# Kernel tuning notes

Measured on AMD Instinct MI355X. Metric: run time of the kernel, lower is better.

The kernel has to match this reference:

```python
import math
import jax, jax.numpy as jnp
import numpy as np

B, T = 2, 2048
D_MODEL, D_HEAD = 2048, 128
N_Q, N_KV = 16, 4
QPG = N_Q // N_KV  # queries per kv group
ROPE_BASE = 10000.0
YARN_SCALE = 4.0
ORIG_MAX_LEN = 4096
BETA_FAST, BETA_SLOW = 32.0, 1.0
RMS_EPS = 1.1920929e-07  # torch.finfo(float32).eps (nn.RMSNorm default)


def _yarn_inv_freq():
    inv = 1.0 / ROPE_BASE ** (np.arange(0, D_HEAD, 2, dtype=np.float32) / D_HEAD)
    wavelengths = 2.0 * math.pi / inv
    low_wavelen = ORIG_MAX_LEN / BETA_SLOW
    high_wavelen = ORIG_MAX_LEN / BETA_FAST
    gamma = np.clip((low_wavelen - wavelengths) / (low_wavelen - high_wavelen), 0.0, 1.0)
    return (gamma * inv + (1.0 - gamma) * inv / YARN_SCALE).astype(np.float32)

INV_FREQ = jnp.asarray(_yarn_inv_freq())  # (D_HEAD//2,) constant buffer
MSCALE = 0.1 * math.log(YARN_SCALE) + 1.0
ATTN_SCALE = 1.0 / (MSCALE * math.sqrt(D_HEAD))


def _rms_norm(x, w):
    # normalize over last dim (d_head), learnable per-dim weight
    return x * jax.lax.rsqrt(jnp.mean(x * x, axis=-1, keepdims=True) + RMS_EPS) * w


def _apply_rope(x):
    # x: (..., T, d_head)
    t = jnp.arange(x.shape[-2], dtype=jnp.float32)
    freqs = jnp.outer(t, INV_FREQ)                 # (T, d/2)
    emb = jnp.concatenate([freqs, freqs], axis=-1)  # (T, d)
    cos, sin = jnp.cos(emb), jnp.sin(emb)
    half = x.shape[-1] // 2
    x_rot = jnp.concatenate([-x[..., half:], x[..., :half]], axis=-1)
    return x * cos + x_rot * sin


def setup_inputs() -> dict:
    key = jax.random.key(0)
    ks = jax.random.split(key, 5)
    x = jax.random.normal(ks[0], (B, T, D_MODEL), dtype=jnp.float32)
    w_scale = 0.02
    Wq = jax.random.normal(ks[1], (D_MODEL, N_Q * D_HEAD), dtype=jnp.float32) * w_scale
    Wkv = jax.random.normal(ks[2], (D_MODEL, 2 * N_KV * D_HEAD), dtype=jnp.float32) * w_scale
    Wo = jax.random.normal(ks[3], (N_Q * D_HEAD, D_MODEL), dtype=jnp.float32) * w_scale
    q_norm_w = jnp.ones((D_HEAD,), dtype=jnp.float32)
    k_norm_w = jnp.ones((D_HEAD,), dtype=jnp.float32)
    return {"x": x, "Wq": Wq, "Wkv": Wkv, "Wo": Wo,
            "q_norm_w": q_norm_w, "k_norm_w": k_norm_w}


def reference(x, Wq, Wkv, Wo, q_norm_w, k_norm_w):
    b, t, _ = x.shape
    # projections
    q = (x @ Wq).reshape(b, t, QPG, N_KV, D_HEAD).transpose(0, 2, 3, 1, 4)  # (b,qpg,g,t,d)
    kv = x @ Wkv
    k, v = jnp.split(kv, 2, axis=-1)
    k = k.reshape(b, t, N_KV, D_HEAD).transpose(0, 2, 1, 3)  # (b,g,t,d)
    v = v.reshape(b, t, N_KV, D_HEAD).transpose(0, 2, 1, 3)  # (b,g,t,d)
    # RMSNorm + YaRN RoPE on q,k (math done in float32 as in source)
    q = _apply_rope(_rms_norm(q, q_norm_w))
    k = _apply_rope(_rms_norm(k, k_norm_w))
    # GQA replication: head index h = qpg*N_KV + g (matches source rearrange/reshape)
    q = q.reshape(b, N_Q, t, D_HEAD)
    k = jnp.broadcast_to(k[:, None], (b, QPG, N_KV, t, D_HEAD)).reshape(b, N_Q, t, D_HEAD)
    v = jnp.broadcast_to(v[:, None], (b, QPG, N_KV, t, D_HEAD)).reshape(b, N_Q, t, D_HEAD)
    # causal SDPA with custom scale
    scores = jnp.einsum('bhtd,bhsd->bhts', q, k) * ATTN_SCALE
    causal = jnp.tril(jnp.ones((t, t), dtype=bool))
    scores = jnp.where(causal, scores, jnp.finfo(scores.dtype).min)
    probs = jax.nn.softmax(scores, axis=-1)
    attn = jnp.einsum('bhts,bhsd->bhtd', probs, v)
    out = attn.transpose(0, 2, 1, 3).reshape(b, t, N_Q * D_HEAD)
    return out @ Wo
```

## Files before the change

kernel.cpp:

```cpp
#include <hip/hip_runtime.h>
#include <cmath>

typedef float f32x4 __attribute__((ext_vector_type(4)));
typedef __bf16 bf16x8 __attribute__((ext_vector_type(8)));

#define DEV static __device__ __forceinline__

DEV unsigned short f2bf(float f) {
  unsigned int u = __builtin_bit_cast(unsigned int, f);
  u += 0x7FFFu + ((u >> 16) & 1u);
  return (unsigned short)(u >> 16);
}
DEV float bf2f(unsigned short h) {
  unsigned int u = ((unsigned int)h) << 16;
  return __builtin_bit_cast(float, u);
}
DEV unsigned int cvtpk(float lo, float hi) {
  unsigned int r;
  asm("v_cvt_pk_bf16_f32 %0, %1, %2" : "=v"(r) : "v"(lo), "v"(hi));
  return r;
}
DEV f32x4 mfma16(bf16x8 a, bf16x8 b, f32x4 c) {
  return __builtin_amdgcn_mfma_f32_16x16x32_bf16(a, b, c, 0, 0, 0);
}
DEV void dma16(const void* g, void* l) {
  __builtin_amdgcn_global_load_lds(
      (const __attribute__((address_space(1))) void*)(uintptr_t)g,
      (__attribute__((address_space(3))) void*)(unsigned int)(uintptr_t)l,
      16, 0, 0);
}

constexpr int T_SEQ = 2048;

__global__ __launch_bounds__(256) void build_rope(float2* __restrict__ rope) {
  int gid = blockIdx.x * 256 + threadIdx.x;
  if (gid >= T_SEQ * 64) return;
  int t = gid >> 6, i = gid & 63;
  double inv = pow(10000.0, -((double)(2 * i)) / 128.0);
  double wl = 6.283185307179586 / inv;
  double gm = (4096.0 - wl) / (4096.0 - 128.0);
  gm = gm < 0.0 ? 0.0 : (gm > 1.0 ? 1.0 : gm);
  float f = (float)(gm * inv + (1.0 - gm) * inv * 0.25);
  float th = (float)t * f;
  float s, c;
  sincosf(th, &s, &c);
  rope[gid] = make_float2(c, s);
}

__global__ __launch_bounds__(256) void cvt_f32_bf16(const float4* __restrict__ in,
                                                    ushort* __restrict__ out, int n4) {
  int i = blockIdx.x * 256 + threadIdx.x;
  if (i >= n4) return;
  float4 v = in[i];
  unsigned int lo = (unsigned int)f2bf(v.x) | ((unsigned int)f2bf(v.y) << 16);
  unsigned int hi = (unsigned int)f2bf(v.z) | ((unsigned int)f2bf(v.w) << 16);
  int row = i >> 9;
  int e = (i * 4) & 2047;
  size_t o = ((size_t)row << 11) + (size_t)(e ^ ((row & 7) << 3));
  *(uint2*)(out + o) = make_uint2(lo, hi);
}

__global__ __launch_bounds__(256) void tconv(const float* __restrict__ in,
                                             ushort* __restrict__ out, int R, int C) {
  __shared__ ushort tile[64][65];
  int c0 = blockIdx.x * 64, r0 = blockIdx.y * 64;
  int j = threadIdx.x & 63, i0 = threadIdx.x >> 6;
#pragma unroll
  for (int ii = 0; ii < 16; ++ii) {
    int i = i0 + ii * 4;
    tile[i][j] = f2bf(in[(size_t)(r0 + i) * C + c0 + j]);
  }
  __syncthreads();
#pragma unroll
  for (int ii = 0; ii < 16; ++ii) {
    int jr = i0 + ii * 4;
    out[(size_t)(c0 + jr) * R + ((r0 + j) ^ ((jr & 7) << 3))] = tile[j][jr];
  }
}

template <int OUT_BF16>
__global__ __launch_bounds__(256) void gemm_bt(const ushort* __restrict__ A,
                                               const ushort* __restrict__ Bt,
                                               void* __restrict__ Cv,
                                               int M, int N, int K) {
  __shared__ ushort lA[128 * 64];
  __shared__ ushort lB[128 * 64];
  const int tid = threadIdx.x;
  const int lane = tid & 63;
  const int w = tid >> 6;
  const int m0 = blockIdx.y * 128;
  const int n0 = blockIdx.x * 128;
  const int wm = (w >> 1) << 6;
  const int wn = (w & 1) << 6;

  f32x4 acc[4][4] = {};

  const size_t K2 = (size_t)K * 2;
  const char* Ab = (const char*)A + (size_t)m0 * K2;
  const char* Bb = (const char*)Bt + (size_t)n0 * K2;
  const int drow = w * 32 + (lane >> 3);
  const int dcb = (lane & 7) * 16;

  for (int k0 = 0; k0 < K; k0 += 64) {
#pragma unroll
    for (int ii = 0; ii < 4; ++ii) {
      const int off = w * 4096 + ii * 1024;
      const size_t gofs = (size_t)(drow + ii * 8) * K2 + (size_t)k0 * 2 + dcb;
      dma16(Ab + gofs, (char*)lA + off);
      dma16(Bb + gofs, (char*)lB + off);
    }
    __syncthreads();
#pragma unroll
    for (int kc = 0; kc < 2; ++kc) {
      bf16x8 a[4], bb[4];
#pragma unroll
      for (int mt = 0; mt < 4; ++mt) {
        int row = wm + mt * 16 + (lane & 15);
        int byo = kc * 64 + ((lane >> 4) << 4);
        a[mt] = *(const bf16x8*)((const char*)lA + row * 128 + (byo ^ ((row & 7) << 4)));
      }
#pragma unroll
      for (int nt = 0; nt < 4; ++nt) {
        int row = wn + nt * 16 + (lane & 15);
        int byo = kc * 64 + ((lane >> 4) << 4);
        bb[nt] = *(const bf16x8*)((const char*)lB + row * 128 + (byo ^ ((row & 7) << 4)));
      }
#pragma unroll
      for (int mt = 0; mt < 4; ++mt)
#pragma unroll
        for (int nt = 0; nt < 4; ++nt)
          acc[mt][nt] = mfma16(a[mt], bb[nt], acc[mt][nt]);
    }
    __syncthreads();
  }

  const int rr = (lane >> 4) << 2;
  const int cc = lane & 15;
  if (OUT_BF16) {
    ushort* C = (ushort*)Cv;
#pragma unroll
    for (int mt = 0; mt < 4; ++mt)
#pragma unroll
      for (int nt = 0; nt < 4; ++nt)
#pragma unroll
        for (int j = 0; j < 4; ++j) {
          int r = m0 + wm + mt * 16 + rr + j;
          int c = n0 + wn + nt * 16 + cc;
          C[(size_t)r * N + c] = f2bf(acc[mt][nt][j]);
        }
  } else {
    float* C = (float*)Cv;
#pragma unroll
    for (int mt = 0; mt < 4; ++mt)
#pragma unroll
      for (int nt = 0; nt < 4; ++nt)
#pragma unroll
        for (int j = 0; j < 4; ++j) {
          int r = m0 + wm + mt * 16 + rr + j;
          int c = n0 + wn + nt * 16 + cc;
          C[(size_t)r * N + c] = acc[mt][nt][j];
        }
  }
}

__global__ __launch_bounds__(256) void norm_rope(const ushort* __restrict__ qkv,
                                                 const float* __restrict__ qw,
                                                 const float* __restrict__ kw,
                                                 const float2* __restrict__ rope,
                                                 ushort* __restrict__ qout,
                                                 ushort* __restrict__ kout,
                                                 float q_scale) {
  const int w = threadIdx.x >> 6, lane = threadIdx.x & 63;
  const int vi = blockIdx.x * 4 + w;
  const ushort* src;
  const float* wt;
  ushort* dst;
  float extra;
  int t, bb;
  if (vi < 65536) {
    int row = vi >> 4, H = vi & 15;
    bb = row >> 11;
    t = row & 2047;
    src = qkv + (size_t)row * 3072 + H * 128 + lane * 2;
    wt = qw;
    extra = q_scale;
    dst = qout + ((size_t)(bb * 16 + H) * T_SEQ + t) * 128 + lane * 2;
  } else {
    int vi2 = vi - 65536;
    int row = vi2 >> 2, gg = vi2 & 3;
    bb = row >> 11;
    t = row & 2047;
    src = qkv + (size_t)row * 3072 + 2048 + gg * 128 + lane * 2;
    wt = kw;
    extra = 1.f;
    dst = kout + ((size_t)(bb * 4 + gg) * T_SEQ + t) * 128 +
          ((lane * 2) ^ ((t & 7) << 3));
  }
  float x0 = bf2f(src[0]), x1 = bf2f(src[1]);
  float ss = x0 * x0 + x1 * x1;
#pragma unroll
  for (int d = 1; d < 64; d <<= 1) ss += __shfl_xor(ss, d, 64);
  float sc = rsqrtf(ss * (1.f / 128.f) + 1.1920929e-7f);
  float w0 = wt[lane * 2], w1 = wt[lane * 2 + 1];
  float xn0 = x0 * sc * w0, xn1 = x1 * sc * w1;
  float p0 = __shfl_xor(xn0, 32, 64), p1 = __shfl_xor(xn1, 32, 64);
  float r0 = lane < 32 ? -p0 : p0;
  float r1 = lane < 32 ? -p1 : p1;
  int i0 = (lane * 2) & 63;
  float2 cs0 = rope[t * 64 + i0];
  float2 cs1 = rope[t * 64 + i0 + 1];
  float o0 = (xn0 * cs0.x + r0 * cs0.y) * extra;
  float o1 = (xn1 * cs1.x + r1 * cs1.y) * extra;
  unsigned int pk = (unsigned int)f2bf(o0) | ((unsigned int)f2bf(o1) << 16);
  *(unsigned int*)dst = pk;
}

__global__ __launch_bounds__(256) void tv_kernel(const ushort* __restrict__ qkv,
                                                 ushort* __restrict__ vt) {
  __shared__ ushort tile[64][65];
  int t0 = blockIdx.x * 64;
  int y = blockIdx.y;
  int dh = y & 1, bg = y >> 1;
  int bb = bg >> 2, g = bg & 3;
  int j = threadIdx.x & 63, i0 = threadIdx.x >> 6;
#pragma unroll
  for (int ii = 0; ii < 16; ++ii) {
    int i = i0 + ii * 4;
    tile[i][j] = qkv[(size_t)(bb * T_SEQ + t0 + i) * 3072 + 2560 + g * 128 + dh * 64 + j];
  }
  __syncthreads();
#pragma unroll
  for (int ii = 0; ii < 16; ++ii) {
    int jr = i0 + ii * 4;
    vt[((size_t)bg * 128 + dh * 64 + jr) * T_SEQ + ((t0 + j) ^ ((jr & 7) << 3))] = tile[j][jr];
  }
}

__global__ __launch_bounds__(256, 2) void attn_fwd(const ushort* __restrict__ qh,
                                                   const ushort* __restrict__ kh,
                                                   const ushort* __restrict__ vt,
                                                   ushort* __restrict__ o) {
  const int f = blockIdx.x;
  const int half = f >> 8, c = f & 255;
  const int kk = c >> 5, bh = c & 31;
  const int qt = half ? kk : (15 - kk);
  const int b = bh >> 4, H = bh & 15;
  const int g = H & 3;
  const int tid = threadIdx.x, lane = tid & 63, w = tid >> 6;
  const int wrow0 = qt * 128 + w * 32;

  __shared__ ushort lK[2][64 * 128];
  __shared__ ushort lV[2][128 * 64];
  __shared__ ushort lP[4 * 32 * 64];

  bf16x8 qf[2][4];
#pragma unroll
  for (int mt = 0; mt < 2; ++mt) {
    const ushort* qb = qh + ((size_t)(b * 16 + H) * T_SEQ + wrow0 + mt * 16 + (lane & 15)) * 128 +
                       ((lane >> 4) << 3);
#pragma unroll
    for (int kc = 0; kc < 4; ++kc) qf[mt][kc] = *(const bf16x8*)(qb + kc * 32);
  }

  f32x4 oacc[2][8] = {};
  float mrow[2] = {-INFINITY, -INFINITY};
  float lrow[2] = {0.f, 0.f};

  const char* kpl = (const char*)(kh + (size_t)(b * 4 + g) * T_SEQ * 128);
  const char* vpl = (const char*)(vt + (size_t)(b * 4 + g) * 128 * T_SEQ);

  auto stage = [&](int j, int bi) {
#pragma unroll
    for (int ii = 0; ii < 4; ++ii) {
      const int off = w * 4096 + ii * 1024;
      dma16(kpl + (size_t)j * 16384 + off + lane * 16, (char*)lK[bi] + off);
      const int vrow = w * 32 + ii * 8 + (lane >> 3);
      dma16(vpl + (size_t)vrow * (T_SEQ * 2) + j * 128 + (lane & 7) * 16,
            (char*)lV[bi] + off);
    }
  };

  stage(0, 0);

  const int rsel = ((lane >> 4) << 2);

  const int jmax = 2 * qt + 1;
  for (int j = 0; j <= jmax; ++j) {
    const int cur = j & 1;
    if (j < jmax) {
      stage(j + 1, cur ^ 1);
      asm volatile("s_waitcnt vmcnt(8)" ::: "memory");
    } else {
      asm volatile("s_waitcnt vmcnt(0)" ::: "memory");
    }
    __builtin_amdgcn_s_barrier();
    __builtin_amdgcn_sched_barrier(0);

    f32x4 s[2][4];
#pragma unroll
    for (int nt = 0; nt < 4; ++nt) {
      bf16x8 kf[4];
      int krow = nt * 16 + (lane & 15);
#pragma unroll
      for (int kc = 0; kc < 4; ++kc) {
        int byo = kc * 64 + ((lane >> 4) << 4);
        kf[kc] = *(const bf16x8*)((const char*)lK[cur] + krow * 256 + (byo ^ ((krow & 7) << 4)));
      }
#pragma unroll
      for (int mt = 0; mt < 2; ++mt) {
        f32x4 a = {0.f, 0.f, 0.f, 0.f};
#pragma unroll
        for (int kc = 0; kc < 4; ++kc) a = mfma16(kf[kc], qf[mt][kc], a);
        s[mt][nt] = a;
      }
    }

    if (j * 64 + 63 > wrow0) {
#pragma unroll
      for (int mt = 0; mt < 2; ++mt) {
        int qrow = wrow0 + mt * 16 + (lane & 15);
#pragma unroll
        for (int nt = 0; nt < 4; ++nt)
#pragma unroll
          for (int jj = 0; jj < 4; ++jj) {
            int col = j * 64 + nt * 16 + rsel + jj;
            if (col > qrow) s[mt][nt][jj] = -3.0e38f;
          }
      }
    }

    float pm[2], mn[2];
#pragma unroll
    for (int mt = 0; mt < 2; ++mt) {
      float a0 = fmaxf(fmaxf(s[mt][0][0], s[mt][0][1]), fmaxf(s[mt][0][2], s[mt][0][3]));
      float a1 = fmaxf(fmaxf(s[mt][1][0], s[mt][1][1]), fmaxf(s[mt][1][2], s[mt][1][3]));
      float a2 = fmaxf(fmaxf(s[mt][2][0], s[mt][2][1]), fmaxf(s[mt][2][2], s[mt][2][3]));
      float a3 = fmaxf(fmaxf(s[mt][3][0], s[mt][3][1]), fmaxf(s[mt][3][2], s[mt][3][3]));
      float p = fmaxf(fmaxf(a0, a1), fmaxf(a2, a3));
      p = fmaxf(p, __shfl_xor(p, 16, 64));
      p = fmaxf(p, __shfl_xor(p, 32, 64));
      pm[mt] = p;
      mn[mt] = mrow[mt];
    }

    bool ok = (pm[0] <= mrow[0] + 11.5417f) && (pm[1] <= mrow[1] + 11.5417f);
    if (!__all(ok)) {
#pragma unroll
      for (int mt = 0; mt < 2; ++mt) {
        mn[mt] = fmaxf(mrow[mt], pm[mt]);
        float rsc = exp2f(mrow[mt] - mn[mt]);
        mrow[mt] = mn[mt];
        lrow[mt] *= rsc;
        float rr0 = __shfl(rsc, rsel + 0, 64);
        float rr1 = __shfl(rsc, rsel + 1, 64);
        float rr2 = __shfl(rsc, rsel + 2, 64);
        float rr3 = __shfl(rsc, rsel + 3, 64);
#pragma unroll
        for (int dt = 0; dt < 8; ++dt) {
          oacc[mt][dt][0] *= rr0; oacc[mt][dt][1] *= rr1;
          oacc[mt][dt][2] *= rr2; oacc[mt][dt][3] *= rr3;
        }
      }
    }

#pragma unroll
    for (int mt = 0; mt < 2; ++mt) {
      float ps = 0.f;
      int prow = mt * 16 + (lane & 15);
      char* pbase = (char*)lP + w * 4096 + prow * 128;
      int swz = (prow & 7) << 4;
#pragma unroll
      for (int nt = 0; nt < 4; ++nt) {
        float p0 = exp2f(s[mt][nt][0] - mn[mt]);
        float p1 = exp2f(s[mt][nt][1] - mn[mt]);
        float p2 = exp2f(s[mt][nt][2] - mn[mt]);
        float p3 = exp2f(s[mt][nt][3] - mn[mt]);
        ps += (p0 + p1) + (p2 + p3);
        int pcb = (nt * 32 + ((lane >> 4) << 3)) ^ swz;
        *(uint2*)(pbase + pcb) = make_uint2(cvtpk(p0, p1), cvtpk(p2, p3));
      }
      ps += __shfl_xor(ps, 16, 64);
      ps += __shfl_xor(ps, 32, 64);
      lrow[mt] += ps;
    }

#pragma unroll
    for (int kc2 = 0; kc2 < 2; ++kc2) {
      bf16x8 pa[2];
#pragma unroll
      for (int mt = 0; mt < 2; ++mt) {
        int prow = mt * 16 + (lane & 15);
        int pbo = kc2 * 64 + ((lane >> 4) << 4);
        pa[mt] = *(const bf16x8*)((char*)lP + w * 4096 + prow * 128 + (pbo ^ ((prow & 7) << 4)));
      }
#pragma unroll
      for (int dt = 0; dt < 8; ++dt) {
        int vrow = dt * 16 + (lane & 15);
        int vbo = kc2 * 64 + ((lane >> 4) << 4);
        bf16x8 vf = *(const bf16x8*)((const char*)lV[cur] + vrow * 128 + (vbo ^ ((vrow & 7) << 4)));
#pragma unroll
        for (int mt = 0; mt < 2; ++mt) oacc[mt][dt] = mfma16(pa[mt], vf, oacc[mt][dt]);
      }
    }

    __builtin_amdgcn_sched_barrier(0);
    __builtin_amdgcn_s_barrier();
  }

#pragma unroll
  for (int mt = 0; mt < 2; ++mt) {
    float linv = 1.f / lrow[mt];
    float iv0 = __shfl(linv, rsel + 0, 64);
    float iv1 = __shfl(linv, rsel + 1, 64);
    float iv2 = __shfl(linv, rsel + 2, 64);
    float iv3 = __shfl(linv, rsel + 3, 64);
    int row = wrow0 + mt * 16 + rsel;
#pragma unroll
    for (int dt = 0; dt < 8; ++dt) {
      int col = H * 128 + dt * 16 + (lane & 15);
      o[(size_t)(b * T_SEQ + row + 0) * 2048 + (col ^ (((row + 0) & 7) << 3))] =
          f2bf(oacc[mt][dt][0] * iv0);
      o[(size_t)(b * T_SEQ + row + 1) * 2048 + (col ^ (((row + 1) & 7) << 3))] =
          f2bf(oacc[mt][dt][1] * iv1);
      o[(size_t)(b * T_SEQ + row + 2) * 2048 + (col ^ (((row + 2) & 7) << 3))] =
          f2bf(oacc[mt][dt][2] * iv2);
      o[(size_t)(b * T_SEQ + row + 3) * 2048 + (col ^ (((row + 3) & 7) << 3))] =
          f2bf(oacc[mt][dt][3] * iv3);
    }
  }
}

extern "C" void kernel_launch(void* const* d_in, const int* in_sizes, int n_in,
                              void* d_out, int out_size, void* d_ws, size_t ws_size,
                              hipStream_t stream) {
  (void)in_sizes; (void)n_in; (void)out_size; (void)ws_size;
  const float* x = (const float*)d_in[0];
  const float* Wq = (const float*)d_in[1];
  const float* Wkv = (const float*)d_in[2];
  const float* Wo = (const float*)d_in[3];
  const float* qnw = (const float*)d_in[4];
  const float* knw = (const float*)d_in[5];
  float* out = (float*)d_out;
  char* ws = (char*)d_ws;

  ushort* xb = (ushort*)(ws);
  ushort* wqkv = (ushort*)(ws + 16777216);
  ushort* wot = (ushort*)(ws + 29360128);
  ushort* qkvraw = (ushort*)(ws + 37748736);
  ushort* kh = (ushort*)(ws + 62914560);
  ushort* vtp = (ushort*)(ws + 67108864);
  float2* rope = (float2*)(ws + 71303168);
  ushort* qh = xb;
  ushort* attnb = qkvraw;

  float attn_scale = 1.0f / ((0.1f * logf(4.0f) + 1.0f) * sqrtf(128.0f));
  float q_scale = attn_scale * 1.44269504f;

  build_rope<<<512, 256, 0, stream>>>(rope);
  cvt_f32_bf16<<<8192, 256, 0, stream>>>((const float4*)x, xb, 2097152);
  tconv<<<dim3(32, 32), 256, 0, stream>>>(Wq, wqkv, 2048, 2048);
  tconv<<<dim3(16, 32), 256, 0, stream>>>(Wkv, wqkv + (size_t)2048 * 2048, 2048, 1024);
  tconv<<<dim3(32, 32), 256, 0, stream>>>(Wo, wot, 2048, 2048);
  gemm_bt<1><<<dim3(24, 32), 256, 0, stream>>>(xb, wqkv, qkvraw, 4096, 3072, 2048);
  norm_rope<<<20480, 256, 0, stream>>>(qkvraw, qnw, knw, rope, qh, kh, q_scale);
  tv_kernel<<<dim3(32, 16), 256, 0, stream>>>(qkvraw, vtp);
  attn_fwd<<<512, 256, 0, stream>>>(qh, kh, vtp, attnb);
  gemm_bt<0><<<dim3(16, 32), 256, 0, stream>>>(attnb, wot, out, 4096, 2048, 2048);
}
```

Baseline: 226.5 us.

## Replace GEMM with larger-tile double-buffered 512-thread kernel

Replaces the 128x128 single-buffered GEMM with a templated kernel using 256-wide N tiles (BM of 256 or 128) and 8 waves per block. LDS is double-buffered so the DMA loads for the next K tile overlap the MFMA work on the current one, gated by explicit vmcnt waits and raw barriers, and s_setprio is raised around the MFMA bursts. The larger tiles improve data reuse per block but use more LDS and registers and launch fewer blocks: 192 for the QKV projection and 256 for the output projection, which may under-fill the 256 CUs. The hardcoded vmcnt counts must match the number of DMA issues per stage.

```diff
diff --git a/kernel.cpp b/kernel.cpp
--- a/kernel.cpp
+++ b/kernel.cpp
@@ -78,60 +78,93 @@
   }
 }
 
-template <int OUT_BF16>
-__global__ __launch_bounds__(256) void gemm_bt(const ushort* __restrict__ A,
+template <int BM, int OUT_BF16>
+__global__ __launch_bounds__(512) void gemm256(const ushort* __restrict__ A,
                                                const ushort* __restrict__ Bt,
                                                void* __restrict__ Cv,
                                                int M, int N, int K) {
-  __shared__ ushort lA[128 * 64];
-  __shared__ ushort lB[128 * 64];
-  const int tid = threadIdx.x;
-  const int lane = tid & 63;
-  const int w = tid >> 6;
-  const int m0 = blockIdx.y * 128;
-  const int n0 = blockIdx.x * 128;
-  const int wm = (w >> 1) << 6;
-  const int wn = (w & 1) << 6;
-
-  f32x4 acc[4][4] = {};
+  constexpr int MT = BM / 32;
+  constexpr int NPH = MT / 2;
+  constexpr int ADMA = BM / 64;
+  __shared__ ushort lA[2][BM * 64];
+  __shared__ ushort lB[2][256 * 64];
+  const int tid = threadIdx.x, lane = tid & 63, w = tid >> 6;
+  const int wm = (w >> 2) * (BM / 2);
+  const int wn = (w & 3) * 64;
+  const int m0 = blockIdx.y * BM, n0 = blockIdx.x * 256;
+
+  f32x4 acc[MT][4] = {};
 
   const size_t K2 = (size_t)K * 2;
   const char* Ab = (const char*)A + (size_t)m0 * K2;
   const char* Bb = (const char*)Bt + (size_t)n0 * K2;
-  const int drow = w * 32 + (lane >> 3);
-  const int dcb = (lane & 7) * 16;
-
-  for (int k0 = 0; k0 < K; k0 += 64) {
+  const int srb = lane >> 3;
+  const int scb = (lane & 7) * 16;
+
+  auto stage = [&](int t, int bi) {
+#pragma unroll
+    for (int ii = 0; ii < ADMA; ++ii) {
+      const int ar = w * (BM / 8) + ii * 8;
+      dma16(Ab + (size_t)(ar + srb) * K2 + (size_t)t * 128 + scb,
+            (char*)lA[bi] + ar * 128);
+    }
 #pragma unroll
     for (int ii = 0; ii < 4; ++ii) {
-      const int off = w * 4096 + ii * 1024;
-      const size_t gofs = (size_t)(drow + ii * 8) * K2 + (size_t)k0 * 2 + dcb;
-      dma16(Ab + gofs, (char*)lA + off);
-      dma16(Bb + gofs, (char*)lB + off);
-    }
-    __syncthreads();
-#pragma unroll
-    for (int kc = 0; kc < 2; ++kc) {
-      bf16x8 a[4], bb[4];
-#pragma unroll
-      for (int mt = 0; mt < 4; ++mt) {
-        int row = wm + mt * 16 + (lane & 15);
-        int byo = kc * 64 + ((lane >> 4) << 4);
-        a[mt] = *(const bf16x8*)((const char*)lA + row * 128 + (byo ^ ((row & 7) << 4)));
-      }
-#pragma unroll
-      for (int nt = 0; nt < 4; ++nt) {
-        int row = wn + nt * 16 + (lane & 15);
-        int byo = kc * 64 + ((lane >> 4) << 4);
-        bb[nt] = *(const bf16x8*)((const char*)lB + row * 128 + (byo ^ ((row & 7) << 4)));
-      }
-#pragma unroll
-      for (int mt = 0; mt < 4; ++mt)
-#pragma unroll
-        for (int nt = 0; nt < 4; ++nt)
-          acc[mt][nt] = mfma16(a[mt], bb[nt], acc[mt][nt]);
-    }
-    __syncthreads();
+      const int br = w * 32 + ii * 8;
+      dma16(Bb + (size_t)(br + srb) * K2 + (size_t)t * 128 + scb,
+            (char*)lB[bi] + br * 128);
+    }
+  };
+
+  stage(0, 0);
+  const int nkt = K >> 6;
+
+  for (int t = 0; t < nkt; ++t) {
+    const int cur = t & 1;
+    if (t + 1 < nkt) {
+      stage(t + 1, cur ^ 1);
+      if constexpr (BM == 256)
+        asm volatile("s_waitcnt vmcnt(8)" ::: "memory");
+      else
+        asm volatile("s_waitcnt vmcnt(6)" ::: "memory");
+    } else {
+      asm volatile("s_waitcnt vmcnt(0)" ::: "memory");
+    }
+    __builtin_amdgcn_s_barrier();
+    __builtin_amdgcn_sched_barrier(0);
+
+    const char* lAc = (const char*)lA[cur];
+    const char* lBc = (const char*)lB[cur];
+
+#pragma unroll
+    for (int ph = 0; ph < NPH; ++ph) {
+      const int mb = (BM == 256) ? (ph >> 1) * 4 : 0;
+      const int nb = (BM == 256) ? (ph & 1) * 2 : ph * 2;
+#pragma unroll
+      for (int kk = 0; kk < 2; ++kk) {
+        bf16x8 af[4], bfr[2];
+        const int byo = kk * 64 + ((lane >> 4) << 4);
+#pragma unroll
+        for (int i = 0; i < 4; ++i) {
+          int row = wm + (mb + i) * 16 + (lane & 15);
+          af[i] = *(const bf16x8*)(lAc + row * 128 + (byo ^ ((row & 7) << 4)));
+        }
+#pragma unroll
+        for (int i = 0; i < 2; ++i) {
+          int row = wn + (nb + i) * 16 + (lane & 15);
+          bfr[i] = *(const bf16x8*)(lBc + row * 128 + (byo ^ ((row & 7) << 4)));
+        }
+        __builtin_amdgcn_s_setprio(1);
+#pragma unroll
+        for (int i = 0; i < 4; ++i)
+#pragma unroll
+          for (int j = 0; j < 2; ++j)
+            acc[mb + i][nb + j] = mfma16(af[i], bfr[j], acc[mb + i][nb + j]);
+        __builtin_amdgcn_s_setprio(0);
+      }
+    }
+    __builtin_amdgcn_sched_barrier(0);
+    __builtin_amdgcn_s_barrier();
   }
 
   const int rr = (lane >> 4) << 2;
@@ -139,7 +172,7 @@
   if (OUT_BF16) {
     ushort* C = (ushort*)Cv;
 #pragma unroll
-    for (int mt = 0; mt < 4; ++mt)
+    for (int mt = 0; mt < MT; ++mt)
 #pragma unroll
       for (int nt = 0; nt < 4; ++nt)
 #pragma unroll
@@ -151,7 +184,7 @@
   } else {
     float* C = (float*)Cv;
 #pragma unroll
-    for (int mt = 0; mt < 4; ++mt)
+    for (int mt = 0; mt < MT; ++mt)
 #pragma unroll
       for (int nt = 0; nt < 4; ++nt)
 #pragma unroll
@@ -461,9 +494,9 @@
   tconv<<<dim3(32, 32), 256, 0, stream>>>(Wq, wqkv, 2048, 2048);
   tconv<<<dim3(16, 32), 256, 0, stream>>>(Wkv, wqkv + (size_t)2048 * 2048, 2048, 1024);
   tconv<<<dim3(32, 32), 256, 0, stream>>>(Wo, wot, 2048, 2048);
-  gemm_bt<1><<<dim3(24, 32), 256, 0, stream>>>(xb, wqkv, qkvraw, 4096, 3072, 2048);
+  gemm256<256, 1><<<dim3(12, 16), 512, 0, stream>>>(xb, wqkv, qkvraw, 4096, 3072, 2048);
   norm_rope<<<20480, 256, 0, stream>>>(qkvraw, qnw, knw, rope, qh, kh, q_scale);
   tv_kernel<<<dim3(32, 16), 256, 0, stream>>>(qkvraw, vtp);
   attn_fwd<<<512, 256, 0, stream>>>(qh, kh, vtp, attnb);
-  gemm_bt<0><<<dim3(16, 32), 256, 0, stream>>>(attnb, wot, out, 4096, 2048, 2048);
-}
+  gemm256<128, 0><<<dim3(8, 32), 512, 0, stream>>>(attnb, wot, out, 4096, 2048, 2048);
+}
```

Measured after the change: 221.2 us. 1.02x faster.
